# Performance work log

Measured on AMD Instinct MI355X. Metric: run time of the kernel, lower is better.

Reference implementation:

```python
import jax, jax.numpy as jnp
import numpy as np

B, T, IN, H, L, OUT = 64, 512, 128, 512, 2, 1


def setup_inputs() -> dict:
    key = jax.random.key(0)
    ks = jax.random.split(key, 4 * L + 3)
    inp = {"X": jax.random.normal(ks[0], (B, T, IN), dtype=jnp.float32)}
    s_in = 1.0 / np.sqrt(H)
    for l in range(L):
        d_in = IN if l == 0 else H
        inp[f"W_ih{l}"] = jax.random.uniform(ks[1 + 4 * l], (3 * H, d_in), minval=-s_in, maxval=s_in, dtype=jnp.float32)
        inp[f"W_hh{l}"] = jax.random.uniform(ks[2 + 4 * l], (3 * H, H), minval=-s_in, maxval=s_in, dtype=jnp.float32)
        inp[f"b_ih{l}"] = jax.random.uniform(ks[3 + 4 * l], (3 * H,), minval=-s_in, maxval=s_in, dtype=jnp.float32)
        inp[f"b_hh{l}"] = jax.random.uniform(ks[4 + 4 * l], (3 * H,), minval=-s_in, maxval=s_in, dtype=jnp.float32)
    s_fc = 1.0 / np.sqrt(H)
    inp["fc_W"] = jax.random.uniform(ks[-2], (OUT, H), minval=-s_fc, maxval=s_fc, dtype=jnp.float32)
    inp["fc_b"] = jax.random.uniform(ks[-1], (OUT,), minval=-s_fc, maxval=s_fc, dtype=jnp.float32)
    return inp


def _gru_layer(x_seq, W_ih, W_hh, b_ih, b_hh):
    # x_seq: [B, T, D_in] -> hidden sequence [B, T, H]
    # Precompute input projections for all timesteps (one big GEMM).
    xg = jnp.einsum('btd,gd->btg', x_seq, W_ih) + b_ih  # [B, T, 3H]
    h0 = jnp.zeros((x_seq.shape[0], W_hh.shape[1]), dtype=x_seq.dtype)

    def step(h, xt):
        hg = h @ W_hh.T + b_hh  # [B, 3H]
        xr, xz, xn = jnp.split(xt, 3, axis=-1)
        hr, hz, hn = jnp.split(hg, 3, axis=-1)
        r = jax.nn.sigmoid(xr + hr)
        z = jax.nn.sigmoid(xz + hz)
        n = jnp.tanh(xn + r * hn)
        h_new = (1.0 - z) * n + z * h
        return h_new, h_new

    _, hs = jax.lax.scan(step, h0, xg.transpose(1, 0, 2))  # hs: [T, B, H]
    return hs.transpose(1, 0, 2)


def reference(X, W_ih0, W_hh0, b_ih0, b_hh0, W_ih1, W_hh1, b_ih1, b_hh1, fc_W, fc_b):
    h = _gru_layer(X, W_ih0, W_hh0, b_ih0, b_hh0)
    h = _gru_layer(h, W_ih1, W_hh1, b_ih1, b_hh1)
    return h[:, -1, :] @ fc_W.T + fc_b  # [B, OUT]
```

## Files before the change

### kernel.cpp

```cpp
#include <hip/hip_runtime.h>


constexpr int Bb = 64, Tt = 512, DIN = 128, Hh = 512;
constexpr int BH = Bb * Hh;
constexpr int S0 = 644;
constexpr int S1 = 1028;
constexpr int PR = 20;

typedef float  f32x4  __attribute__((ext_vector_type(4)));
typedef short  bf16x8 __attribute__((ext_vector_type(8)));
typedef int    i32x4  __attribute__((ext_vector_type(4)));
typedef unsigned long long u64;

#define MFMA16 __builtin_amdgcn_mfma_f32_16x16x32_bf16

__device__ __forceinline__ unsigned rne_bf16(unsigned xb){
    return (xb + 0x7FFFu + ((xb >> 16) & 1u)) >> 16;
}
__device__ __forceinline__ unsigned pack_split(float x){
    unsigned hb = rne_bf16(__float_as_uint(x));
    float hf = __uint_as_float(hb << 16);
    unsigned lb = rne_bf16(__float_as_uint(x - hf));
    return (hb << 16) | lb;
}
__device__ __forceinline__ float unpack_f32(unsigned u){
    return __uint_as_float(u & 0xFFFF0000u) + __uint_as_float(u << 16);
}

union FragU { unsigned w[4]; bf16x8 v; };

__device__ __forceinline__ void make_wfrag(const float* p, bf16x8& wh, bf16x8& wl){
    FragU hi, lo;
#pragma unroll
    for (int i = 0; i < 4; ++i){
        unsigned pa = pack_split(p[2*i]), pb = pack_split(p[2*i+1]);
        hi.w[i] = (pa >> 16) | (pb & 0xFFFF0000u);
        lo.w[i] = (pa & 0xFFFFu) | (pb << 16);
    }
    wh = hi.v; wl = lo.v;
}
__device__ __forceinline__ void make_afrag(const unsigned* u, bf16x8& ah, bf16x8& al){
    FragU hi, lo;
#pragma unroll
    for (int i = 0; i < 4; ++i){
        unsigned a = u[2*i], b = u[2*i+1];
        hi.w[i] = __builtin_amdgcn_perm(b, a, 0x07060302u);
        lo.w[i] = __builtin_amdgcn_perm(b, a, 0x05040100u);
    }
    ah = hi.v; al = lo.v;
}

__device__ __forceinline__ u64 ald64(const u64* p){
    return __hip_atomic_load(p, __ATOMIC_RELAXED, __HIP_MEMORY_SCOPE_AGENT);
}
__device__ __forceinline__ void ast64(u64* p, u64 v){
    __hip_atomic_store(p, v, __ATOMIC_RELAXED, __HIP_MEMORY_SCOPE_AGENT);
}

__device__ __forceinline__ bool bad4(const i32x4& v, unsigned tag){
    unsigned x = ((unsigned)v[0] ^ tag) | ((unsigned)v[1] ^ tag)
               | ((unsigned)v[2] ^ tag) | ((unsigned)v[3] ^ tag);
    return (x & 1u) != 0u;
}
__device__ __forceinline__ void fix4(const unsigned* p, unsigned tag, i32x4& v){
    if (bad4(v, tag)){
        for (;;){
            u64 a = ald64((const u64*)p);
            u64 b = ald64((const u64*)p + 1);
            v[0] = (int)(unsigned)a; v[1] = (int)(unsigned)(a >> 32);
            v[2] = (int)(unsigned)b; v[3] = (int)(unsigned)(b >> 32);
            if (!bad4(v, tag)) break;
            __builtin_amdgcn_s_sleep(1);
        }
    }
}

template<bool BIG>
__global__ __launch_bounds__(512, 1) void gru_main(
    const float* __restrict__ X,
    const float* __restrict__ Wih0, const float* __restrict__ Whh0,
    const float* __restrict__ bih0, const float* __restrict__ bhh0,
    const float* __restrict__ Wih1, const float* __restrict__ Whh1,
    const float* __restrict__ bih1, const float* __restrict__ bhh1,
    const float* __restrict__ fcW, const float* __restrict__ fcb,
    float* __restrict__ out,
    unsigned* hseq0, unsigned* hseq1)
{
    __builtin_amdgcn_fence(__ATOMIC_ACQUIRE, "agent");

    __shared__ unsigned Alds[16 * S1];
    __shared__ float P[8][3][16 * PR];
    __shared__ unsigned hout[256];

    const int tid  = threadIdx.x;
    const int lane = tid & 63;
    const int w    = tid >> 6;
    const bool isL1 = blockIdx.x >= 128;
    const int lb = isL1 ? (int)blockIdx.x - 128 : (int)blockIdx.x;
    const int m  = lb >> 5;
    const int cb = lb & 31;
    const int c0 = cb * 16;
    const int STR  = isL1 ? S1 : S0;
    const int HOFF = isL1 ? 512 : 128;

    const bool active = isL1 || (w < 5);

    bf16x8 whi[4][3], wlo[4][3];
    if (active){
        const int n = lane & 15;
#pragma unroll
        for (int ks = 0; ks < 4; ++ks){
            int kq = w * 128 + ks * 32 + (lane >> 4) * 8;
            const float* src; long kloc, rowlen;
            if (isL1){
                if (kq < 512){ src = Wih1; kloc = kq; } else { src = Whh1; kloc = kq - 512; }
                rowlen = 512;
            } else {
                if (kq < 128){ src = Wih0; kloc = kq; rowlen = 128; }
                else         { src = Whh0; kloc = kq - 128; rowlen = 512; }
            }
#pragma unroll
            for (int g = 0; g < 3; ++g){
                long row = (long)g * Hh + c0 + n;
                make_wfrag(src + row * rowlen + kloc, whi[ks][g], wlo[ks][g]);
            }
        }
    }
    float Br = 0.f, Bz = 0.f, Bin = 0.f, Bhn = 0.f;
    if (tid < 256){
        int c = c0 + (tid & 15);
        const float* bi = isL1 ? bih1 : bih0;
        const float* bh = isL1 ? bhh1 : bhh0;
        Br  = bi[c] + bh[c];
        Bz  = bi[Hh + c] + bh[Hh + c];
        Bin = bi[2*Hh + c];
        Bhn = bh[2*Hh + c];
    }

    for (int t = 0; t < Tt; ++t){
        if (isL1){
            const unsigned* s0 = hseq0 + ((long)t * Bb + m*16) * (long)Hh;
            long r1 = BIG ? (long)(t-1) * BH : (long)((t-1) & 1) * BH;
            const unsigned* s1 = hseq1 + r1 + (long)(m*16) * Hh;
            unsigned tag1 = BIG ? 1u : (1u - (((unsigned)(t-1) >> 1) & 1u));
            const unsigned* a0[4]; const unsigned* a1[4];
            i32x4 v0[4], v1[4];
#pragma unroll
            for (int it = 0; it < 4; ++it){
                int j = it*512 + tid; int row = j >> 7, col = (j & 127) * 4;
                a0[it] = s0 + (long)row * Hh + col;
                v0[it] = *(const i32x4*)a0[it];
            }
            if (t > 0){
#pragma unroll
                for (int it = 0; it < 4; ++it){
                    int j = it*512 + tid; int row = j >> 7, col = (j & 127) * 4;
                    a1[it] = s1 + (long)row * Hh + col;
                    v1[it] = *(const i32x4*)a1[it];
                }
            }
#pragma unroll
            for (int it = 0; it < 4; ++it) fix4(a0[it], 1u, v0[it]);
            if (t > 0){
#pragma unroll
                for (int it = 0; it < 4; ++it) fix4(a1[it], tag1, v1[it]);
            } else {
#pragma unroll
                for (int it = 0; it < 4; ++it) v1[it] = i32x4{0,0,0,0};
            }
#pragma unroll
            for (int it = 0; it < 4; ++it){
                int j = it*512 + tid; int row = j >> 7, col = (j & 127) * 4;
                *(i32x4*)(Alds + row * S1 + col) = v0[it];
                *(i32x4*)(Alds + row * S1 + 512 + col) = v1[it];
            }
        } else {
            {
                int row = tid >> 5, c4 = (tid & 31) * 4;
                f32x4 xv = *(const f32x4*)(X + ((long)(m*16 + row) * Tt + t) * DIN + c4);
                i32x4 pv;
                pv[0] = (int)pack_split(xv[0]);
                pv[1] = (int)pack_split(xv[1]);
                pv[2] = (int)pack_split(xv[2]);
                pv[3] = (int)pack_split(xv[3]);
                *(i32x4*)(Alds + row * S0 + c4) = pv;
            }
            if (t > 0){
                const unsigned* s0 = hseq0 + ((long)(t-1) * Bb + m*16) * (long)Hh;
                const unsigned* a0[4]; i32x4 v0[4];
#pragma unroll
                for (int it = 0; it < 4; ++it){
                    int j = it*512 + tid; int row = j >> 7, col = (j & 127) * 4;
                    a0[it] = s0 + (long)row * Hh + col;
                    v0[it] = *(const i32x4*)a0[it];
                }
#pragma unroll
                for (int it = 0; it < 4; ++it) fix4(a0[it], 1u, v0[it]);
#pragma unroll
                for (int it = 0; it < 4; ++it){
                    int j = it*512 + tid; int row = j >> 7, col = (j & 127) * 4;
                    *(i32x4*)(Alds + row * S0 + 128 + col) = v0[it];
                }
            } else {
#pragma unroll
                for (int it = 0; it < 8; ++it){
                    int j = it*512 + tid;
                    *(u64*)(Alds + (j >> 8) * S0 + 128 + (j & 255) * 2) = 0ULL;
                }
            }
        }
        __syncthreads();

        if (active){
            f32x4 a0 = {0.f,0.f,0.f,0.f}, a1 = a0, a2 = a0;
            const unsigned* arow = Alds + (lane & 15) * STR + w * 128 + (lane >> 4) * 8;
#pragma unroll
            for (int ks = 0; ks < 4; ++ks){
                unsigned uu[8];
                *(i32x4*)&uu[0] = *(const i32x4*)(arow + ks*32);
                *(i32x4*)&uu[4] = *(const i32x4*)(arow + ks*32 + 4);
                bf16x8 ah, al; make_afrag(uu, ah, al);
                a0 = MFMA16(ah, whi[ks][0], a0, 0,0,0);
                a0 = MFMA16(ah, wlo[ks][0], a0, 0,0,0);
                a0 = MFMA16(al, whi[ks][0], a0, 0,0,0);
                a1 = MFMA16(ah, whi[ks][1], a1, 0,0,0);
                a1 = MFMA16(ah, wlo[ks][1], a1, 0,0,0);
                a1 = MFMA16(al, whi[ks][1], a1, 0,0,0);
                a2 = MFMA16(ah, whi[ks][2], a2, 0,0,0);
                a2 = MFMA16(ah, wlo[ks][2], a2, 0,0,0);
                a2 = MFMA16(al, whi[ks][2], a2, 0,0,0);
            }
            int q = lane >> 4, n = lane & 15;
#pragma unroll
            for (int r4 = 0; r4 < 4; ++r4){
                int idx = (q*4 + r4)*PR + n;
                P[w][0][idx] = a0[r4];
                P[w][1][idx] = a1[r4];
                P[w][2][idx] = a2[r4];
            }
        }
        __syncthreads();

        unsigned wtag = isL1 ? (BIG ? 1u : (1u - (((unsigned)t >> 1) & 1u))) : 1u;
        if (tid < 256){
            int bm = tid >> 4, n = tid & 15;
            int idx = bm * PR + n;
            float sr, sz, snx, snh;
            if (isL1){
                sr  = P[0][0][idx]+P[1][0][idx]+P[2][0][idx]+P[3][0][idx]
                    + P[4][0][idx]+P[5][0][idx]+P[6][0][idx]+P[7][0][idx];
                sz  = P[0][1][idx]+P[1][1][idx]+P[2][1][idx]+P[3][1][idx]
                    + P[4][1][idx]+P[5][1][idx]+P[6][1][idx]+P[7][1][idx];
                snx = P[0][2][idx]+P[1][2][idx]+P[2][2][idx]+P[3][2][idx];
                snh = P[4][2][idx]+P[5][2][idx]+P[6][2][idx]+P[7][2][idx];
            } else {
                sr  = P[0][0][idx]+P[1][0][idx]+P[2][0][idx]+P[3][0][idx]+P[4][0][idx];
                sz  = P[0][1][idx]+P[1][1][idx]+P[2][1][idx]+P[3][1][idx]+P[4][1][idx];
                snx = P[0][2][idx];
                snh = P[1][2][idx]+P[2][2][idx]+P[3][2][idx]+P[4][2][idx];
            }
            float r  = 1.f/(1.f + __expf(-(sr + Br)));
            float z  = 1.f/(1.f + __expf(-(sz + Bz)));
            float ee = __expf(2.f*(snx + Bin + r*(snh + Bhn)));
            float nn = 1.f - 2.f/(ee + 1.f);
            float hp = unpack_f32(Alds[bm*STR + HOFF + c0 + n]);
            float hnew = (1.f - z)*nn + z*hp;
            hout[tid] = (pack_split(hnew) & ~1u) | wtag;
        }
        __syncthreads();

        if (tid < 128){
            int bm = tid >> 3, k = (tid & 7) * 2;
            u64 v = (u64)hout[bm*16 + k] | ((u64)hout[bm*16 + k + 1] << 32);
            unsigned* base = isL1
                ? hseq1 + (BIG ? (long)t * BH : (long)(t & 1) * BH)
                : hseq0 + (long)t * BH;
            ast64((u64*)(base + (long)(m*16 + bm) * Hh + c0 + k), v);
        }
    }

    if (isL1 && cb == 31){
        unsigned ftag = BIG ? 1u : (1u - (((unsigned)(Tt-1) >> 1) & 1u));
        const unsigned* hb = hseq1 + (BIG ? (long)(Tt-1) * BH : (long)((Tt-1) & 1) * BH);
        int half = lane >> 5, l5 = lane & 31;
        int b = m*16 + w*2 + half;
        const u64* hrow = (const u64*)(hb + (long)b * Hh);
        float p = 0.f;
#pragma unroll
        for (int i = 0; i < 8; ++i){
            int k = l5 + 32*i;
            u64 v = ald64(hrow + k);
            while (((((unsigned)v ^ ftag) | ((unsigned)(v >> 32) ^ ftag)) & 1u) != 0u){
                __builtin_amdgcn_s_sleep(1);
                v = ald64(hrow + k);
            }
            p += unpack_f32((unsigned)v) * fcW[2*k]
               + unpack_f32((unsigned)(v >> 32)) * fcW[2*k+1];
        }
#pragma unroll
        for (int off = 16; off > 0; off >>= 1) p += __shfl_xor(p, off);
        if (l5 == 0) out[b] = p + fcb[0];
    }
}

extern "C" void kernel_launch(void* const* d_in, const int* in_sizes, int n_in,
                              void* d_out, int out_size, void* d_ws, size_t ws_size,
                              hipStream_t stream) {
    const float* X    = (const float*)d_in[0];
    const float* Wih0 = (const float*)d_in[1];
    const float* Whh0 = (const float*)d_in[2];
    const float* bih0 = (const float*)d_in[3];
    const float* bhh0 = (const float*)d_in[4];
    const float* Wih1 = (const float*)d_in[5];
    const float* Whh1 = (const float*)d_in[6];
    const float* bih1 = (const float*)d_in[7];
    const float* bhh1 = (const float*)d_in[8];
    const float* fcW  = (const float*)d_in[9];
    const float* fcb  = (const float*)d_in[10];
    float* out = (float*)d_out;

    unsigned* hseq0 = (unsigned*)d_ws;
    unsigned* hseq1 = hseq0 + (long)Tt * BH;
    size_t need_big = (size_t)2 * Tt * BH * 4;
    bool big = ws_size >= need_big;

    if (big)
        gru_main<true><<<256, 512, 0, stream>>>(X, Wih0, Whh0, bih0, bhh0,
                                                Wih1, Whh1, bih1, bhh1, fcW, fcb,
                                                out, hseq0, hseq1);
    else
        gru_main<false><<<256, 512, 0, stream>>>(X, Wih0, Whh0, bih0, bhh0,
                                                 Wih1, Whh1, bih1, bhh1, fcW, fcb,
                                                 out, hseq0, hseq1);
}
```

Before: 1.723 ms.

## Load recurrent A fragments straight into registers, dropping LDS staging and a barrier

Each active wave now loads its own MFMA A-fragment slice (hidden state or packed X) directly from global memory into registers, instead of the whole block staging rows into a shared LDS tile. This removes the LDS A buffer, one __syncthreads per timestep and the hout staging buffer. The previous hidden value is kept in a register as full fp32 rather than re-read from LDS. Results are written with per-element 32-bit atomic stores instead of 64-bit packed stores. The trade-offs are more, narrower global stores and per-wave global loads with tag polling on the serial critical path.

```diff
diff --git a/kernel.cpp b/kernel.cpp
--- a/kernel.cpp
+++ b/kernel.cpp
@@ -3,8 +3,6 @@
 
 constexpr int Bb = 64, Tt = 512, DIN = 128, Hh = 512;
 constexpr int BH = Bb * Hh;
-constexpr int S0 = 644;
-constexpr int S1 = 1028;
 constexpr int PR = 20;
 
 typedef float  f32x4  __attribute__((ext_vector_type(4)));
@@ -53,7 +51,7 @@
 __device__ __forceinline__ u64 ald64(const u64* p){
     return __hip_atomic_load(p, __ATOMIC_RELAXED, __HIP_MEMORY_SCOPE_AGENT);
 }
-__device__ __forceinline__ void ast64(u64* p, u64 v){
+__device__ __forceinline__ void ast32(unsigned* p, unsigned v){
     __hip_atomic_store(p, v, __ATOMIC_RELAXED, __HIP_MEMORY_SCOPE_AGENT);
 }
 
@@ -88,9 +86,7 @@
 {
     __builtin_amdgcn_fence(__ATOMIC_ACQUIRE, "agent");
 
-    __shared__ unsigned Alds[16 * S1];
     __shared__ float P[8][3][16 * PR];
-    __shared__ unsigned hout[256];
 
     const int tid  = threadIdx.x;
     const int lane = tid & 63;
@@ -100,17 +96,15 @@
     const int m  = lb >> 5;
     const int cb = lb & 31;
     const int c0 = cb * 16;
-    const int STR  = isL1 ? S1 : S0;
-    const int HOFF = isL1 ? 512 : 128;
 
     const bool active = isL1 || (w < 5);
+    const int r = lane & 15, q = lane >> 4;
 
     bf16x8 whi[4][3], wlo[4][3];
     if (active){
-        const int n = lane & 15;
 #pragma unroll
         for (int ks = 0; ks < 4; ++ks){
-            int kq = w * 128 + ks * 32 + (lane >> 4) * 8;
+            int kq = w * 128 + ks * 32 + q * 8;
             const float* src; long kloc, rowlen;
             if (isL1){
                 if (kq < 512){ src = Wih1; kloc = kq; } else { src = Whh1; kloc = kq - 512; }
@@ -120,9 +114,9 @@
                 else         { src = Whh0; kloc = kq - 128; rowlen = 512; }
             }
 #pragma unroll
-            for (int g = 0; g < 3; ++g){
-                long row = (long)g * Hh + c0 + n;
-                make_wfrag(src + row * rowlen + kloc, whi[ks][g], wlo[ks][g]);
+            for (int g2 = 0; g2 < 3; ++g2){
+                long row = (long)g2 * Hh + c0 + r;
+                make_wfrag(src + row * rowlen + kloc, whi[ks][g2], wlo[ks][g2]);
             }
         }
     }
@@ -137,88 +131,88 @@
         Bhn = bh[2*Hh + c];
     }
 
+    float hp = 0.f;
+
     for (int t = 0; t < Tt; ++t){
-        if (isL1){
-            const unsigned* s0 = hseq0 + ((long)t * Bb + m*16) * (long)Hh;
-            long r1 = BIG ? (long)(t-1) * BH : (long)((t-1) & 1) * BH;
-            const unsigned* s1 = hseq1 + r1 + (long)(m*16) * Hh;
-            unsigned tag1 = BIG ? 1u : (1u - (((unsigned)(t-1) >> 1) & 1u));
-            const unsigned* a0[4]; const unsigned* a1[4];
-            i32x4 v0[4], v1[4];
-#pragma unroll
-            for (int it = 0; it < 4; ++it){
-                int j = it*512 + tid; int row = j >> 7, col = (j & 127) * 4;
-                a0[it] = s0 + (long)row * Hh + col;
-                v0[it] = *(const i32x4*)a0[it];
-            }
-            if (t > 0){
-#pragma unroll
-                for (int it = 0; it < 4; ++it){
-                    int j = it*512 + tid; int row = j >> 7, col = (j & 127) * 4;
-                    a1[it] = s1 + (long)row * Hh + col;
-                    v1[it] = *(const i32x4*)a1[it];
+        if (active){
+            i32x4 av[8];
+            const unsigned* ap[8];
+            unsigned atag = 1u;
+            bool have = true;
+
+            if (isL1){
+                const unsigned* s0 = hseq0 + ((long)t * Bb + m*16) * (long)Hh;
+                long r1 = BIG ? (long)(t-1) * BH : (long)((t-1) & 1) * BH;
+                const unsigned* s1 = hseq1 + r1 + (long)(m*16) * Hh;
+                unsigned tag1 = BIG ? 1u : (1u - (((unsigned)(t-1) >> 1) & 1u));
+                if (w < 4){
+#pragma unroll
+                    for (int ks = 0; ks < 4; ++ks){
+                        int C = w*128 + q*8 + ks*32;
+                        ap[ks*2]   = s0 + (long)r * Hh + C;
+                        ap[ks*2+1] = ap[ks*2] + 4;
+                    }
+                    atag = 1u;
+                } else {
+#pragma unroll
+                    for (int ks = 0; ks < 4; ++ks){
+                        int C = (w-4)*128 + q*8 + ks*32;
+                        ap[ks*2]   = s1 + (long)r * Hh + C;
+                        ap[ks*2+1] = ap[ks*2] + 4;
+                    }
+                    atag = tag1;
+                    if (t == 0) have = false;
                 }
-            }
-#pragma unroll
-            for (int it = 0; it < 4; ++it) fix4(a0[it], 1u, v0[it]);
-            if (t > 0){
-#pragma unroll
-                for (int it = 0; it < 4; ++it) fix4(a1[it], tag1, v1[it]);
-            } else {
-#pragma unroll
-                for (int it = 0; it < 4; ++it) v1[it] = i32x4{0,0,0,0};
-            }
-#pragma unroll
-            for (int it = 0; it < 4; ++it){
-                int j = it*512 + tid; int row = j >> 7, col = (j & 127) * 4;
-                *(i32x4*)(Alds + row * S1 + col) = v0[it];
-                *(i32x4*)(Alds + row * S1 + 512 + col) = v1[it];
-            }
-        } else {
-            {
-                int row = tid >> 5, c4 = (tid & 31) * 4;
-                f32x4 xv = *(const f32x4*)(X + ((long)(m*16 + row) * Tt + t) * DIN + c4);
-                i32x4 pv;
-                pv[0] = (int)pack_split(xv[0]);
-                pv[1] = (int)pack_split(xv[1]);
-                pv[2] = (int)pack_split(xv[2]);
-                pv[3] = (int)pack_split(xv[3]);
-                *(i32x4*)(Alds + row * S0 + c4) = pv;
-            }
-            if (t > 0){
-                const unsigned* s0 = hseq0 + ((long)(t-1) * Bb + m*16) * (long)Hh;
-                const unsigned* a0[4]; i32x4 v0[4];
-#pragma unroll
-                for (int it = 0; it < 4; ++it){
-                    int j = it*512 + tid; int row = j >> 7, col = (j & 127) * 4;
-                    a0[it] = s0 + (long)row * Hh + col;
-                    v0[it] = *(const i32x4*)a0[it];
-                }
-#pragma unroll
-                for (int it = 0; it < 4; ++it) fix4(a0[it], 1u, v0[it]);
-#pragma unroll
-                for (int it = 0; it < 4; ++it){
-                    int j = it*512 + tid; int row = j >> 7, col = (j & 127) * 4;
-                    *(i32x4*)(Alds + row * S0 + 128 + col) = v0[it];
+                if (have){
+#pragma unroll
+                    for (int i = 0; i < 8; ++i) av[i] = *(const i32x4*)ap[i];
+#pragma unroll
+                    for (int i = 0; i < 8; ++i) fix4(ap[i], atag, av[i]);
+                } else {
+#pragma unroll
+                    for (int i = 0; i < 8; ++i) av[i] = i32x4{0,0,0,0};
                 }
             } else {
-#pragma unroll
-                for (int it = 0; it < 8; ++it){
-                    int j = it*512 + tid;
-                    *(u64*)(Alds + (j >> 8) * S0 + 128 + (j & 255) * 2) = 0ULL;
+                if (w == 0){
+                    const float* xb = X + ((long)(m*16 + r) * Tt + t) * DIN;
+#pragma unroll
+                    for (int ks = 0; ks < 4; ++ks){
+                        int C = q*8 + ks*32;
+                        f32x4 x0 = *(const f32x4*)(xb + C);
+                        f32x4 x1 = *(const f32x4*)(xb + C + 4);
+                        i32x4 p0, p1;
+                        p0[0] = (int)pack_split(x0[0]); p0[1] = (int)pack_split(x0[1]);
+                        p0[2] = (int)pack_split(x0[2]); p0[3] = (int)pack_split(x0[3]);
+                        p1[0] = (int)pack_split(x1[0]); p1[1] = (int)pack_split(x1[1]);
+                        p1[2] = (int)pack_split(x1[2]); p1[3] = (int)pack_split(x1[3]);
+                        av[ks*2] = p0; av[ks*2+1] = p1;
+                    }
+                } else {
+                    const unsigned* s0 = hseq0 + ((long)(t-1) * Bb + m*16) * (long)Hh;
+#pragma unroll
+                    for (int ks = 0; ks < 4; ++ks){
+                        int C = (w-1)*128 + q*8 + ks*32;
+                        ap[ks*2]   = s0 + (long)r * Hh + C;
+                        ap[ks*2+1] = ap[ks*2] + 4;
+                    }
+                    if (t == 0){
+#pragma unroll
+                        for (int i = 0; i < 8; ++i) av[i] = i32x4{0,0,0,0};
+                    } else {
+#pragma unroll
+                        for (int i = 0; i < 8; ++i) av[i] = *(const i32x4*)ap[i];
+#pragma unroll
+                        for (int i = 0; i < 8; ++i) fix4(ap[i], 1u, av[i]);
+                    }
                 }
             }
-        }
-        __syncthreads();
-
-        if (active){
+
             f32x4 a0 = {0.f,0.f,0.f,0.f}, a1 = a0, a2 = a0;
-            const unsigned* arow = Alds + (lane & 15) * STR + w * 128 + (lane >> 4) * 8;
 #pragma unroll
             for (int ks = 0; ks < 4; ++ks){
                 unsigned uu[8];
-                *(i32x4*)&uu[0] = *(const i32x4*)(arow + ks*32);
-                *(i32x4*)&uu[4] = *(const i32x4*)(arow + ks*32 + 4);
+                *(i32x4*)&uu[0] = av[ks*2];
+                *(i32x4*)&uu[4] = av[ks*2+1];
                 bf16x8 ah, al; make_afrag(uu, ah, al);
                 a0 = MFMA16(ah, whi[ks][0], a0, 0,0,0);
                 a0 = MFMA16(ah, wlo[ks][0], a0, 0,0,0);
@@ -230,10 +224,9 @@
                 a2 = MFMA16(ah, wlo[ks][2], a2, 0,0,0);
                 a2 = MFMA16(al, whi[ks][2], a2, 0,0,0);
             }
-            int q = lane >> 4, n = lane & 15;
 #pragma unroll
             for (int r4 = 0; r4 < 4; ++r4){
-                int idx = (q*4 + r4)*PR + n;
+                int idx = (q*4 + r4)*PR + r;
                 P[w][0][idx] = a0[r4];
                 P[w][1][idx] = a1[r4];
                 P[w][2][idx] = a2[r4];
@@ -259,24 +252,19 @@
                 snx = P[0][2][idx];
                 snh = P[1][2][idx]+P[2][2][idx]+P[3][2][idx]+P[4][2][idx];
             }
-            float r  = 1.f/(1.f + __expf(-(sr + Br)));
+            float rg = 1.f/(1.f + __expf(-(sr + Br)));
             float z  = 1.f/(1.f + __expf(-(sz + Bz)));
-            float ee = __expf(2.f*(snx + Bin + r*(snh + Bhn)));
+            float ee = __expf(2.f*(snx + Bin + rg*(snh + Bhn)));
             float nn = 1.f - 2.f/(ee + 1.f);
-            float hp = unpack_f32(Alds[bm*STR + HOFF + c0 + n]);
             float hnew = (1.f - z)*nn + z*hp;
-            hout[tid] = (pack_split(hnew) & ~1u) | wtag;
-        }
-        __syncthreads();
-
-        if (tid < 128){
-            int bm = tid >> 3, k = (tid & 7) * 2;
-            u64 v = (u64)hout[bm*16 + k] | ((u64)hout[bm*16 + k + 1] << 32);
+            hp = hnew;
+            unsigned pv = (pack_split(hnew) & ~1u) | wtag;
             unsigned* base = isL1
                 ? hseq1 + (BIG ? (long)t * BH : (long)(t & 1) * BH)
                 : hseq0 + (long)t * BH;
-            ast64((u64*)(base + (long)(m*16 + bm) * Hh + c0 + k), v);
-        }
+            ast32(base + (long)(m*16 + bm) * Hh + c0 + n, pv);
+        }
+        __syncthreads();
     }
 
     if (isL1 && cb == 31){
```

Measured after the change: 1.935 ms. 12.3% more time.
